# Kernel optimization log

Measured on AMD Instinct MI355X. Metric: run time of the kernel, lower is better.

Reference implementation:

```python
import jax, jax.numpy as jnp
import numpy as np

B, T, D = 2, 2048, 1024
N_HEADS = 16
HEAD_DIM = D // N_HEADS


def setup_inputs() -> dict:
    key = jax.random.key(0)
    ks = jax.random.split(key, 5)
    s = 0.02
    return {
        "x": jax.random.normal(ks[0], (B, T, D), jnp.float32),
        "wq": jax.random.normal(ks[1], (D, D), jnp.float32) * s,
        "wk": jax.random.normal(ks[2], (D, D), jnp.float32) * s,
        "wv": jax.random.normal(ks[3], (D, D), jnp.float32) * s,
        "wo": jax.random.normal(ks[4], (D, D), jnp.float32) * s,
        "bo": jnp.zeros((D,), jnp.float32),
    }


def reference(x, wq, wk, wv, wo, bo):
    b, t, _ = x.shape
    # QKV projections (weights stored [d_in, d_out]); reshape to (b, heads, t, head_dim)
    def split_heads(y):
        return y.reshape(b, t, N_HEADS, HEAD_DIM).transpose(0, 2, 1, 3)
    q = split_heads(x @ wq)
    k = split_heads(x @ wk)
    v = split_heads(x @ wv)
    # causal attention scores: (b, h, t, t)
    scores = jnp.einsum("bhqd,bhkd->bhqk", q, k)
    causal = jnp.tril(jnp.ones((t, t), bool))  # True where attending allowed
    scores = jnp.where(causal, scores, -jnp.inf)
    attn = jax.nn.softmax(scores / np.sqrt(HEAD_DIM).astype(np.float32), axis=-1)
    # dropout_rate = 0.0 (eval mode) -> identity
    ctx = jnp.einsum("bhqk,bhkd->bhqd", attn, v)
    ctx = ctx.transpose(0, 2, 1, 3).reshape(b, t, D)
    return ctx @ wo + bo
```

## Files before the change

kernel.cpp:

```cpp
#include <hip/hip_runtime.h>
#include <hip/hip_bf16.h>
#include <cstdint>

typedef __hip_bfloat16 bf16;
typedef __bf16 bf16x8 __attribute__((ext_vector_type(8)));
typedef __bf16 bf16x4 __attribute__((ext_vector_type(4)));
typedef float f32x4 __attribute__((ext_vector_type(4)));
typedef uint32_t u32x4 __attribute__((ext_vector_type(4)));

#define LOG2E 1.4426950408889634f

__device__ __forceinline__ void gload_lds16(const void* g, void* l) {
  __builtin_amdgcn_global_load_lds(
      (const __attribute__((address_space(1))) unsigned int*)g,
      (__attribute__((address_space(3))) unsigned int*)l,
      16, 0, 0);
}

__device__ __forceinline__ uint32_t pack_bf16(float a, float b) {
  const uint32_t ha = (uint32_t)__builtin_bit_cast(uint16_t, (__bf16)a);
  const uint32_t hb = (uint32_t)__builtin_bit_cast(uint16_t, (__bf16)b);
  return ha | (hb << 16);
}

__global__ void conv_k(const float* __restrict__ src, bf16* __restrict__ dst, int n) {
  const int i = (blockIdx.x * 256 + threadIdx.x) * 8;
  if (i >= n) return;
  const f32x4 a = *(const f32x4*)(src + i);
  const f32x4 b = *(const f32x4*)(src + i + 4);
  bf16x8 o;
#pragma unroll
  for (int j = 0; j < 4; ++j) { o[j] = (__bf16)a[j]; o[4 + j] = (__bf16)b[j]; }
  *(bf16x8*)(dst + i) = o;
}

__global__ void transpose_conv4(
    const float* __restrict__ wq, const float* __restrict__ wk,
    const float* __restrict__ wv, const float* __restrict__ wo,
    bf16* __restrict__ dqkv, bf16* __restrict__ dout) {
  __shared__ float tile[32][33];
  const int z = blockIdx.z;
  const float* src = (z == 0) ? wq : ((z == 1) ? wk : ((z == 2) ? wv : wo));
  bf16* dst = (z < 3) ? (dqkv + (long)z * 1048576) : dout;
  const int bx = blockIdx.x * 32, by = blockIdx.y * 32;
  const int tx = threadIdx.x;
  for (int j = threadIdx.y; j < 32; j += 8)
    tile[j][tx] = src[(long)(by + j) * 1024 + bx + tx];
  __syncthreads();
  for (int j = threadIdx.y; j < 32; j += 8)
    dst[(long)(bx + j) * 1024 + by + tx] = __float2bfloat16(tile[tx][j]);
}

__global__ __launch_bounds__(256, 3) void gemm_qkv(
    const bf16* __restrict__ A, const bf16* __restrict__ Bt,
    bf16* __restrict__ Cq, bf16* __restrict__ Ck, bf16* __restrict__ Cv,
    int M, int N, int K) {
  __shared__ __align__(16) bf16 As[128 * 64];
  __shared__ __align__(16) bf16 Bs[128 * 64];

  const int tid = threadIdx.x;
  const int lane = tid & 63;
  const int wave = tid >> 6;
  const int quad = lane >> 4;
  const int l16 = lane & 15;
  const int id = (int)blockIdx.y * 24 + (int)blockIdx.x;
  const int xcd = id & 7, idx = id >> 3;
  const int bxn = xcd * 3 + idx % 3;
  const int byn = idx / 3;
  const int m0 = byn * 128;
  const int n0 = bxn * 128;
  const int wm = (wave >> 1) * 64;
  const int wn = (wave & 1) * 64;

  const f32x4 zero4 = {0.f, 0.f, 0.f, 0.f};
  f32x4 acc[4][4];
#pragma unroll
  for (int mi = 0; mi < 4; ++mi)
#pragma unroll
    for (int ni = 0; ni < 4; ++ni) acc[mi][ni] = zero4;

  const int sRow = tid >> 3;
  const int sK = (tid & 7) * 8;
  const int sSwz = sK ^ (8 * (sRow & 7));
  const bf16* Ag = A + (long)(m0 + sRow) * K + sSwz;
  const bf16* Bg = Bt + (long)(n0 + sRow) * K + sSwz;
  const int swzr = 8 * (l16 & 7);

  for (int k0 = 0; k0 < K; k0 += 64) {
#pragma unroll
    for (int j = 0; j < 4; ++j) {
      gload_lds16(Ag + k0 + (long)(32 * j) * K, &As[tid * 8 + 2048 * j]);
      gload_lds16(Bg + k0 + (long)(32 * j) * K, &Bs[tid * 8 + 2048 * j]);
    }
    __syncthreads();

#pragma unroll
    for (int ks = 0; ks < 64; ks += 32) {
      const int colr = (ks + quad * 8) ^ swzr;
      bf16x8 af[4], bfv[4];
#pragma unroll
      for (int mi = 0; mi < 4; ++mi)
        af[mi] = *(const bf16x8*)&As[(wm + mi * 16 + l16) * 64 + colr];
#pragma unroll
      for (int ni = 0; ni < 4; ++ni)
        bfv[ni] = *(const bf16x8*)&Bs[(wn + ni * 16 + l16) * 64 + colr];
#pragma unroll
      for (int mi = 0; mi < 4; ++mi)
#pragma unroll
        for (int ni = 0; ni < 4; ++ni)
          acc[mi][ni] = __builtin_amdgcn_mfma_f32_16x16x32_bf16(af[mi], bfv[ni], acc[mi][ni], 0, 0, 0);
    }
    __syncthreads();
  }

#pragma unroll
  for (int mi = 0; mi < 4; ++mi) {
    const int gmb = m0 + wm + mi * 16 + quad * 4;
#pragma unroll
    for (int ni = 0; ni < 4; ++ni) {
      const int n = n0 + wn + ni * 16 + l16;
      const int which = n >> 10, rem = n & 1023;
      const int h = rem >> 6, hd = rem & 63;
      bf16* dst = (which == 0) ? Cq : ((which == 1) ? Ck : Cv);
#pragma unroll
      for (int r = 0; r < 4; ++r) {
        const int gm = gmb + r;
        const int b = gm >> 11, t = gm & 2047;
        dst[(((long)(b * 16 + h)) * 2048 + t) * 64 + hd] = __float2bfloat16(acc[mi][ni][r]);
      }
    }
  }
}

__global__ __launch_bounds__(256, 3) void gemm_out(
    const bf16* __restrict__ A, const bf16* __restrict__ Bt,
    const float* __restrict__ bias, float* __restrict__ Cout,
    int M, int N, int K) {
  __shared__ __align__(16) bf16 As[64 * 64];
  __shared__ __align__(16) bf16 Bs[128 * 64];

  const int tid = threadIdx.x;
  const int lane = tid & 63;
  const int wave = tid >> 6;
  const int quad = lane >> 4;
  const int l16 = lane & 15;
  const int id = (int)blockIdx.y * 8 + (int)blockIdx.x;
  const int m0 = (id >> 3) * 64;
  const int n0 = (id & 7) * 128;
  const int wm = (wave & 1) * 32;
  const int wn = (wave >> 1) * 64;

  const f32x4 zero4 = {0.f, 0.f, 0.f, 0.f};
  f32x4 acc[2][4];
#pragma unroll
  for (int mi = 0; mi < 2; ++mi)
#pragma unroll
    for (int ni = 0; ni < 4; ++ni) acc[mi][ni] = zero4;

  const int sRow = tid >> 3;
  const int sK = (tid & 7) * 8;
  const int sSwz = sK ^ (8 * (sRow & 7));
  const bf16* Ag = A + (long)(m0 + sRow) * K + sSwz;
  const bf16* Bg = Bt + (long)(n0 + sRow) * K + sSwz;
  const int swzr = 8 * (l16 & 7);

  for (int k0 = 0; k0 < K; k0 += 64) {
#pragma unroll
    for (int j = 0; j < 2; ++j)
      gload_lds16(Ag + k0 + (long)(32 * j) * K, &As[tid * 8 + 2048 * j]);
#pragma unroll
    for (int j = 0; j < 4; ++j)
      gload_lds16(Bg + k0 + (long)(32 * j) * K, &Bs[tid * 8 + 2048 * j]);
    __syncthreads();

#pragma unroll
    for (int ks = 0; ks < 64; ks += 32) {
      const int colr = (ks + quad * 8) ^ swzr;
      bf16x8 af[2], bfv[4];
#pragma unroll
      for (int mi = 0; mi < 2; ++mi)
        af[mi] = *(const bf16x8*)&As[(wm + mi * 16 + l16) * 64 + colr];
#pragma unroll
      for (int ni = 0; ni < 4; ++ni)
        bfv[ni] = *(const bf16x8*)&Bs[(wn + ni * 16 + l16) * 64 + colr];
#pragma unroll
      for (int mi = 0; mi < 2; ++mi)
#pragma unroll
        for (int ni = 0; ni < 4; ++ni)
          acc[mi][ni] = __builtin_amdgcn_mfma_f32_16x16x32_bf16(af[mi], bfv[ni], acc[mi][ni], 0, 0, 0);
    }
    __syncthreads();
  }

#pragma unroll
  for (int mi = 0; mi < 2; ++mi) {
    const int gmb = m0 + wm + mi * 16 + quad * 4;
#pragma unroll
    for (int ni = 0; ni < 4; ++ni) {
      const int n = n0 + wn + ni * 16 + l16;
      const float bv = bias[n];
#pragma unroll
      for (int r = 0; r < 4; ++r)
        Cout[(long)(gmb + r) * N + n] = acc[mi][ni][r] + bv;
    }
  }
}

__global__ __launch_bounds__(256, 3) void attn_kernel(
    const bf16* __restrict__ Q, const bf16* __restrict__ Kg, const bf16* __restrict__ Vg,
    bf16* __restrict__ ctx) {
  constexpr int KSTR = 72, VSTR = 136;
  __shared__ __align__(16) bf16 Ks[128 * KSTR];
  __shared__ __align__(16) bf16 Vt[64 * VSTR];

  const int tid = threadIdx.x;
  const int lane = tid & 63;
  const int wave = tid >> 6;
  const int quad = lane >> 4;
  const int l16 = lane & 15;

  const int id = (int)blockIdx.y * 16 + (int)blockIdx.x;
  const int g = id & 7;
  const int bh = g * 4 + ((id >> 3) & 3);
  const int p = id >> 5;

  const long base = (long)bh * 2048 * 64;
  const int b = bh >> 4, h = bh & 15;

  const int krow = tid >> 1;
  const int kc32 = (tid & 1) * 32;
  const int vr4 = (tid & 31) * 4;
  const int vd8 = (tid >> 5) * 8;
  const int vb4 = (vr4 >> 4) & 1;
  const int vc4 = (vr4 & ~31) + 8 * (((vr4 >> 2) & 3) ^ vb4) + 4 * vb4;

  const float negsh = -12.0f * LOG2E;
  const f32x4 zero4 = {0.f, 0.f, 0.f, 0.f};

#pragma unroll 1
  for (int seg = 0; seg < 2; ++seg) {
    const int qt = seg ? (31 - p) : p;
    const int qbase = qt * 64 + wave * 16;
    const int q = qbase + l16;

    bf16x8 qf0 = *(const bf16x8*)(Q + base + (long)(qbase + l16) * 64 + quad * 8);
    bf16x8 qf1 = *(const bf16x8*)(Q + base + (long)(qbase + l16) * 64 + 32 + quad * 8);
#pragma unroll
    for (int j = 0; j < 8; ++j) {
      qf0[j] = (__bf16)((float)qf0[j] * 0.125f);
      qf1[j] = (__bf16)((float)qf1[j] * 0.125f);
    }

    float l_i = 0.f;
    f32x4 oacc[4];
#pragma unroll
    for (int nb = 0; nb < 4; ++nb) oacc[nb] = zero4;

    const int nk = (qt + 2) >> 1;
    bf16x8 kr[4], vv[4];
    {
      const bf16* kp = Kg + base + (long)krow * 64 + kc32;
#pragma unroll
      for (int i = 0; i < 4; ++i) kr[i] = *(const bf16x8*)(kp + i * 8);
#pragma unroll
      for (int i = 0; i < 4; ++i)
        vv[i] = *(const bf16x8*)(Vg + base + (long)(vr4 + i) * 64 + vd8);
    }

    for (int kt = 0; kt < nk; ++kt) {
      const int k0 = kt * 128;
#pragma unroll
      for (int i = 0; i < 4; ++i)
        *(bf16x8*)&Ks[krow * KSTR + kc32 + i * 8] = kr[i];
#pragma unroll
      for (int j = 0; j < 8; ++j) {
        bf16x4 t;
        t[0] = vv[0][j]; t[1] = vv[1][j]; t[2] = vv[2][j]; t[3] = vv[3][j];
        *(bf16x4*)&Vt[(vd8 + j) * VSTR + vc4] = t;
      }
      __syncthreads();
      if (kt + 1 < nk) {
        const bf16* kp = Kg + base + (long)(k0 + 128 + krow) * 64 + kc32;
#pragma unroll
        for (int i = 0; i < 4; ++i) kr[i] = *(const bf16x8*)(kp + i * 8);
#pragma unroll
        for (int i = 0; i < 4; ++i)
          vv[i] = *(const bf16x8*)(Vg + base + (long)(k0 + 128 + vr4 + i) * 64 + vd8);
      }

      f32x4 s8[8];
      __builtin_amdgcn_s_setprio(1);
#pragma unroll
      for (int kb = 0; kb < 8; ++kb) {
        const bf16x8 kb0 = *(const bf16x8*)&Ks[(kb * 16 + l16) * KSTR + quad * 8];
        const bf16x8 kb1 = *(const bf16x8*)&Ks[(kb * 16 + l16) * KSTR + 32 + quad * 8];
        f32x4 a = zero4;
        a = __builtin_amdgcn_mfma_f32_16x16x32_bf16(kb0, qf0, a, 0, 0, 0);
        a = __builtin_amdgcn_mfma_f32_16x16x32_bf16(kb1, qf1, a, 0, 0, 0);
        s8[kb] = a;
      }
      __builtin_amdgcn_s_setprio(0);

      if (kt == nk - 1) {
        const int qg = q - k0 - quad * 4;
#pragma unroll
        for (int kb = 0; kb < 8; ++kb)
#pragma unroll
          for (int r = 0; r < 4; ++r)
            s8[kb][r] = (kb * 16 + r <= qg) ? s8[kb][r] : -1e30f;
      }

      float rsum = 0.f;
      u32x4 paw[4];
#pragma unroll
      for (int kk = 0; kk < 4; ++kk) {
        const float p0 = exp2f(fmaf(s8[2 * kk][0], LOG2E, negsh));
        const float p1 = exp2f(fmaf(s8[2 * kk][1], LOG2E, negsh));
        const float p2 = exp2f(fmaf(s8[2 * kk][2], LOG2E, negsh));
        const float p3 = exp2f(fmaf(s8[2 * kk][3], LOG2E, negsh));
        const float p4 = exp2f(fmaf(s8[2 * kk + 1][0], LOG2E, negsh));
        const float p5 = exp2f(fmaf(s8[2 * kk + 1][1], LOG2E, negsh));
        const float p6 = exp2f(fmaf(s8[2 * kk + 1][2], LOG2E, negsh));
        const float p7 = exp2f(fmaf(s8[2 * kk + 1][3], LOG2E, negsh));
        rsum += ((p0 + p1) + (p2 + p3)) + ((p4 + p5) + (p6 + p7));
        u32x4 w;
        w[0] = pack_bf16(p0, p1);
        w[1] = pack_bf16(p2, p3);
        w[2] = (uint32_t)__shfl_xor((int)pack_bf16(p4, p5), 16);
        w[3] = (uint32_t)__shfl_xor((int)pack_bf16(p6, p7), 16);
        paw[kk] = w;
      }

      __builtin_amdgcn_s_setprio(1);
#pragma unroll
      for (int kk = 0; kk < 4; ++kk) {
        const bf16x8 pa = __builtin_bit_cast(bf16x8, paw[kk]);
#pragma unroll
        for (int nb2 = 0; nb2 < 4; ++nb2) {
          const bf16x8 vb = *(const bf16x8*)&Vt[(nb2 * 16 + l16) * VSTR + kk * 32 + quad * 8];
          oacc[nb2] = __builtin_amdgcn_mfma_f32_16x16x32_bf16(pa, vb, oacc[nb2], 0, 0, 0);
        }
      }
      __builtin_amdgcn_s_setprio(0);

      rsum += __shfl_xor(rsum, 16);
      rsum += __shfl_xor(rsum, 32);
      l_i += rsum;
      __syncthreads();
    }

    float linv[4];
#pragma unroll
    for (int r = 0; r < 4; ++r) linv[r] = 1.0f / __shfl(l_i, quad * 4 + r);
#pragma unroll
    for (int r = 0; r < 4; ++r) {
      const int t = qbase + quad * 4 + r;
#pragma unroll
      for (int nb2 = 0; nb2 < 4; ++nb2) {
        const int d = h * 64 + nb2 * 16 + l16;
        ctx[((long)b * 2048 + t) * 1024 + d] = __float2bfloat16(oacc[nb2][r] * linv[r]);
      }
    }
  }
}

extern "C" void kernel_launch(void* const* d_in, const int* in_sizes, int n_in,
                              void* d_out, int out_size, void* d_ws, size_t ws_size,
                              hipStream_t stream) {
  const float* x  = (const float*)d_in[0];
  const float* wq = (const float*)d_in[1];
  const float* wk = (const float*)d_in[2];
  const float* wv = (const float*)d_in[3];
  const float* wo = (const float*)d_in[4];
  const float* bo = (const float*)d_in[5];
  float* out = (float*)d_out;

  bf16* Wtqkv = (bf16*)d_ws;
  bf16* Wto   = Wtqkv + 3145728;
  bf16* xb    = Wto + 1048576;
  bf16* Qb    = xb + 4194304;
  bf16* Kb    = Qb + 4194304;
  bf16* Vb    = Kb + 4194304;
  bf16* Cx    = xb;

  hipLaunchKernelGGL(conv_k, dim3(2048), dim3(256), 0, stream, x, xb, 4194304);
  hipLaunchKernelGGL(transpose_conv4, dim3(32, 32, 4), dim3(32, 8), 0, stream,
                     wq, wk, wv, wo, Wtqkv, Wto);

  hipLaunchKernelGGL(gemm_qkv, dim3(24, 32), dim3(256), 0, stream,
                     xb, Wtqkv, Qb, Kb, Vb, 4096, 3072, 1024);

  hipLaunchKernelGGL(attn_kernel, dim3(16, 32), dim3(256), 0, stream, Qb, Kb, Vb, Cx);

  hipLaunchKernelGGL(gemm_out, dim3(8, 64), dim3(256), 0, stream,
                     Cx, Wto, bo, out, 4096, 1024, 1024);
}
```

Measured before the change: 182.4 us.

## Merge prep kernels and retile QKV GEMM to 128x96 tiles

```diff
diff --git a/kernel.cpp b/kernel.cpp
--- a/kernel.cpp
+++ b/kernel.cpp
@@ -23,31 +23,34 @@
   return ha | (hb << 16);
 }
 
-__global__ void conv_k(const float* __restrict__ src, bf16* __restrict__ dst, int n) {
-  const int i = (blockIdx.x * 256 + threadIdx.x) * 8;
-  if (i >= n) return;
-  const f32x4 a = *(const f32x4*)(src + i);
-  const f32x4 b = *(const f32x4*)(src + i + 4);
-  bf16x8 o;
-#pragma unroll
-  for (int j = 0; j < 4; ++j) { o[j] = (__bf16)a[j]; o[4 + j] = (__bf16)b[j]; }
-  *(bf16x8*)(dst + i) = o;
-}
-
-__global__ void transpose_conv4(
+__global__ __launch_bounds__(256) void prep(
+    const float* __restrict__ x, bf16* __restrict__ xb,
     const float* __restrict__ wq, const float* __restrict__ wk,
     const float* __restrict__ wv, const float* __restrict__ wo,
     bf16* __restrict__ dqkv, bf16* __restrict__ dout) {
   __shared__ float tile[32][33];
-  const int z = blockIdx.z;
+  const int bid = blockIdx.x;
+  if (bid < 2048) {
+    const int i = (bid * 256 + threadIdx.x) * 8;
+    const f32x4 a = *(const f32x4*)(x + i);
+    const f32x4 b = *(const f32x4*)(x + i + 4);
+    bf16x8 o;
+#pragma unroll
+    for (int j = 0; j < 4; ++j) { o[j] = (__bf16)a[j]; o[4 + j] = (__bf16)b[j]; }
+    *(bf16x8*)(xb + i) = o;
+    return;
+  }
+  const int id = bid - 2048;
+  const int z = id >> 10;
+  const int t2 = id & 1023;
+  const int bx = (t2 & 31) * 32, by = (t2 >> 5) * 32;
+  const int tx = threadIdx.x & 31, ty = threadIdx.x >> 5;
   const float* src = (z == 0) ? wq : ((z == 1) ? wk : ((z == 2) ? wv : wo));
   bf16* dst = (z < 3) ? (dqkv + (long)z * 1048576) : dout;
-  const int bx = blockIdx.x * 32, by = blockIdx.y * 32;
-  const int tx = threadIdx.x;
-  for (int j = threadIdx.y; j < 32; j += 8)
+  for (int j = ty; j < 32; j += 8)
     tile[j][tx] = src[(long)(by + j) * 1024 + bx + tx];
   __syncthreads();
-  for (int j = threadIdx.y; j < 32; j += 8)
+  for (int j = ty; j < 32; j += 8)
     dst[(long)(bx + j) * 1024 + by + tx] = __float2bfloat16(tile[tx][j]);
 }
 
@@ -56,28 +59,28 @@
     bf16* __restrict__ Cq, bf16* __restrict__ Ck, bf16* __restrict__ Cv,
     int M, int N, int K) {
   __shared__ __align__(16) bf16 As[128 * 64];
-  __shared__ __align__(16) bf16 Bs[128 * 64];
+  __shared__ __align__(16) bf16 Bs[96 * 64];
 
   const int tid = threadIdx.x;
   const int lane = tid & 63;
   const int wave = tid >> 6;
   const int quad = lane >> 4;
   const int l16 = lane & 15;
-  const int id = (int)blockIdx.y * 24 + (int)blockIdx.x;
+  const int id = (int)blockIdx.y * 32 + (int)blockIdx.x;
   const int xcd = id & 7, idx = id >> 3;
-  const int bxn = xcd * 3 + idx % 3;
-  const int byn = idx / 3;
+  const int bxn = xcd * 4 + (idx & 3);
+  const int byn = idx >> 2;
   const int m0 = byn * 128;
-  const int n0 = bxn * 128;
+  const int n0 = bxn * 96;
   const int wm = (wave >> 1) * 64;
-  const int wn = (wave & 1) * 64;
+  const int wn = (wave & 1) * 48;
 
   const f32x4 zero4 = {0.f, 0.f, 0.f, 0.f};
-  f32x4 acc[4][4];
+  f32x4 acc[4][3];
 #pragma unroll
   for (int mi = 0; mi < 4; ++mi)
 #pragma unroll
-    for (int ni = 0; ni < 4; ++ni) acc[mi][ni] = zero4;
+    for (int ni = 0; ni < 3; ++ni) acc[mi][ni] = zero4;
 
   const int sRow = tid >> 3;
   const int sK = (tid & 7) * 8;
@@ -88,26 +91,27 @@
 
   for (int k0 = 0; k0 < K; k0 += 64) {
 #pragma unroll
-    for (int j = 0; j < 4; ++j) {
+    for (int j = 0; j < 4; ++j)
       gload_lds16(Ag + k0 + (long)(32 * j) * K, &As[tid * 8 + 2048 * j]);
+#pragma unroll
+    for (int j = 0; j < 3; ++j)
       gload_lds16(Bg + k0 + (long)(32 * j) * K, &Bs[tid * 8 + 2048 * j]);
-    }
     __syncthreads();
 
 #pragma unroll
     for (int ks = 0; ks < 64; ks += 32) {
       const int colr = (ks + quad * 8) ^ swzr;
-      bf16x8 af[4], bfv[4];
+      bf16x8 af[4], bfv[3];
 #pragma unroll
       for (int mi = 0; mi < 4; ++mi)
         af[mi] = *(const bf16x8*)&As[(wm + mi * 16 + l16) * 64 + colr];
 #pragma unroll
-      for (int ni = 0; ni < 4; ++ni)
+      for (int ni = 0; ni < 3; ++ni)
         bfv[ni] = *(const bf16x8*)&Bs[(wn + ni * 16 + l16) * 64 + colr];
 #pragma unroll
       for (int mi = 0; mi < 4; ++mi)
 #pragma unroll
-        for (int ni = 0; ni < 4; ++ni)
+        for (int ni = 0; ni < 3; ++ni)
           acc[mi][ni] = __builtin_amdgcn_mfma_f32_16x16x32_bf16(af[mi], bfv[ni], acc[mi][ni], 0, 0, 0);
     }
     __syncthreads();
@@ -117,7 +121,7 @@
   for (int mi = 0; mi < 4; ++mi) {
     const int gmb = m0 + wm + mi * 16 + quad * 4;
 #pragma unroll
-    for (int ni = 0; ni < 4; ++ni) {
+    for (int ni = 0; ni < 3; ++ni) {
       const int n = n0 + wn + ni * 16 + l16;
       const int which = n >> 10, rem = n & 1023;
       const int h = rem >> 6, hd = rem & 63;
@@ -383,11 +387,10 @@
   bf16* Vb    = Kb + 4194304;
   bf16* Cx    = xb;
 
-  hipLaunchKernelGGL(conv_k, dim3(2048), dim3(256), 0, stream, x, xb, 4194304);
-  hipLaunchKernelGGL(transpose_conv4, dim3(32, 32, 4), dim3(32, 8), 0, stream,
-                     wq, wk, wv, wo, Wtqkv, Wto);
-
-  hipLaunchKernelGGL(gemm_qkv, dim3(24, 32), dim3(256), 0, stream,
+  hipLaunchKernelGGL(prep, dim3(6144), dim3(256), 0, stream,
+                     x, xb, wq, wk, wv, wo, Wtqkv, Wto);
+
+  hipLaunchKernelGGL(gemm_qkv, dim3(32, 32), dim3(256), 0, stream,
                      xb, Wtqkv, Qb, Kb, Vb, 4096, 3072, 1024);
 
   hipLaunchKernelGGL(attn_kernel, dim3(16, 32), dim3(256), 0, stream, Qb, Kb, Vb, Cx);
```

After: 176.7 us. -3.1%, faster.
